# Kernel tuning notes

Measured on AMD Instinct MI355X. Metric: run time of the kernel, lower is better.

The kernel has to match this reference:

```python
import jax, jax.numpy as jnp
import numpy as np

# Frankenstein DNC dims (from __init__ defaults, L reduced 16->8 for memory budget)
X = 47764; H = 128; L = 8; VT = 3620; W = 32; R = 8; N = 512; BS = 1
D = X + R * W + 2 * H            # RNN_Unit input width = 48276
ET = W * R + 3 * W + 5 * R + 3   # interface width = 395
EPS = 1e-8


def setup_inputs() -> dict:
    key = jax.random.key(0)
    ks = jax.random.split(key, 16)
    su = 1.0 / np.sqrt(H)          # nn.Linear default-style scale
    sv = 1.0 / np.sqrt(VT)
    se = 1.0 / np.sqrt(ET)
    u = lambda k, shp, s: jax.random.uniform(k, shp, jnp.float32, -s, s)
    return {
        'x_in': jax.random.normal(ks[0], (BS, X), jnp.float32),
        # stacked per-layer LSTM-gate weights (L, D, H) / biases (L, H)
        'W_i': u(ks[1], (L, D, H), su), 'b_i': u(ks[2], (L, H), su),
        'W_f': u(ks[3], (L, D, H), su), 'b_f': u(ks[4], (L, H), su),
        'W_o': u(ks[5], (L, D, H), su), 'b_o': u(ks[6], (L, H), su),
        'W_s': u(ks[7], (L, D, H), su), 'b_s': u(ks[8], (L, H), su),
        'W_y': u(ks[9], (L * H, VT), sv),
        'W_E': u(ks[10], (L * H, ET), se),
        'W_r': u(ks[11], (W * R, VT), sv),
        # memory / state buffers (requires_grad=False in torch)
        'memory': jax.random.uniform(ks[12], (N, W), jnp.float32, -1.0, 1.0),
        'last_read_vector': jnp.zeros((BS, W, R), jnp.float32),
        'hidden_prev': jnp.zeros((BS, L, H), jnp.float32),
        'old_states': jnp.zeros((L, BS, H), jnp.float32),
        'precedence': jnp.zeros((BS, N), jnp.float32),
        'linkage': jnp.zeros((BS, N, N), jnp.float32),
        'last_read_weightings': jnp.zeros((BS, N, R), jnp.float32),
        'last_usage': jnp.zeros((BS, N), jnp.float32),
        'last_write_weighting': jnp.zeros((BS, N), jnp.float32),
    }


def reference(x_in, W_i, b_i, W_f, b_f, W_o, b_o, W_s, b_s, W_y, W_E, W_r,
              memory, last_read_vector, hidden_prev, old_states, precedence,
              linkage, last_read_weightings, last_usage, last_write_weighting):
    # ---- controller: L stacked LSTM-like units, sequential over layers ----
    input_x_t = jnp.concatenate([x_in, last_read_vector.reshape(BS, -1)], axis=1)
    hpt = jnp.transpose(hidden_prev, (1, 0, 2))  # (L, BS, H)

    def layer(h_prev_layer, xs):
        Wi, bi, Wf, bf, Wo, bo, Ws, bs_, hp, os_ = xs
        si = jnp.concatenate([input_x_t, hp, h_prev_layer], axis=1)  # (BS, D)
        ig = jax.nn.sigmoid(si @ Wi + bi)
        fg = jax.nn.sigmoid(si @ Wf + bf)
        st = fg * os_ + ig * jnp.tanh(si @ Ws + bs_)
        og = jax.nn.sigmoid(si @ Wo + bo)
        h = og * jnp.tanh(st)
        return h, h

    _, hs = jax.lax.scan(layer, jnp.zeros((BS, H), x_in.dtype),
                         (W_i, b_i, W_f, b_f, W_o, b_o, W_s, b_s, hpt, old_states))
    flat = jnp.transpose(hs, (1, 0, 2)).reshape(BS, L * H)
    output = flat @ W_y
    E = flat @ W_E

    # ---- interface vector parsing ----
    i0 = 0
    read_keys = E[:, :W * R].reshape(BS, W, R); i0 = W * R
    read_strengths = 1.0 - jax.nn.log_sigmoid(E[:, i0:i0 + R]); i0 += R
    write_key = E[:, i0:i0 + W]; i0 += W
    write_strength = 1.0 - jax.nn.log_sigmoid(E[:, i0:i0 + 1]); i0 += 1
    erase = jax.nn.sigmoid(E[:, i0:i0 + W]); i0 += W
    write_vec = E[:, i0:i0 + W]; i0 += W
    free_gates = jax.nn.sigmoid(E[:, i0:i0 + R]); i0 += R
    alloc_gate = jax.nn.sigmoid(E[:, i0:i0 + 1]); i0 += 1
    write_gate = jax.nn.sigmoid(E[:, i0:i0 + 1]); i0 += 1
    read_modes = jax.nn.softmax(E[:, i0:i0 + 3 * R].reshape(BS, R, 3), axis=2)

    # ---- memory retention, usage, allocation ----
    psi = jnp.prod(1.0 - free_gates[:, None, :] * last_read_weightings, axis=2)  # (BS,N)
    usage = (last_usage + last_write_weighting - last_usage * last_write_weighting) * psi
    idx = jnp.argsort(usage, axis=1)
    su = jnp.take_along_axis(usage, idx, axis=1)
    cp = jnp.cumprod(su, axis=1)
    excl = jnp.concatenate([jnp.ones((BS, 1), usage.dtype), cp[:, :-1]], axis=1)
    alloc = jnp.take_along_axis((1.0 - su) * excl, jnp.argsort(idx, axis=1), axis=1)

    # ---- write weighting (content + allocation) ----
    Mn = memory / jnp.maximum(jnp.linalg.norm(memory, axis=1, keepdims=True), EPS)
    kn = write_key / jnp.maximum(jnp.linalg.norm(write_key, axis=1, keepdims=True), EPS)
    cw = jax.nn.softmax(write_strength * (kn @ Mn.T), axis=1)  # (BS,N)
    ww = write_gate * (alloc_gate * alloc + (1.0 - alloc_gate) * cw)

    # ---- write to memory (bs == 1) ----
    memory_new = memory * (1.0 - jnp.einsum('bn,bw->nw', ww, erase)) \
                 + jnp.einsum('bn,bw->nw', ww, write_vec)

    # ---- temporal linkage ----
    Lm = (1.0 - ww[:, :, None] - ww[:, None, :]) * linkage \
         + ww[:, :, None] * precedence[:, None, :]
    Lm = Lm * (1.0 - jnp.eye(N, dtype=Lm.dtype))[None]
    fw = jnp.einsum('bij,bjr->bir', Lm, last_read_weightings)   # forward weighting
    bw = jnp.einsum('bji,bjr->bir', Lm, last_read_weightings)   # backward weighting

    # ---- read weightings and read vectors ----
    Mn2 = memory_new / jnp.maximum(jnp.linalg.norm(memory_new, axis=1, keepdims=True), EPS)
    knr = read_keys / jnp.maximum(jnp.linalg.norm(read_keys, axis=1, keepdims=True), EPS)
    cr = jax.nn.softmax(read_strengths[:, None, :] * jnp.einsum('nw,bwr->bnr', Mn2, knr), axis=1)
    rw = bw * read_modes[:, None, :, 0] + cr * read_modes[:, None, :, 1] \
         + fw * read_modes[:, None, :, 2]                        # (BS,N,R)
    rv = jnp.einsum('nw,bnr->bwr', memory_new, rw)               # (BS,W,R)

    y = output + rv.reshape(BS, W * R) @ W_r                     # (BS, v_t)
    return y
```

## Files before the change

kernel.cpp:

```cpp
#include <hip/hip_runtime.h>
#include <math.h>

#define XDIM 47764
#define HDIM 128
#define LDIM 8
#define VTDIM 3620
#define WDIM 32
#define RDIM 8
#define NDIM 512
#define RW 256
#define DDIM 48276
#define FIXED 48148
#define ETDIM 395
#define EPSV 1e-8f

#define CHUNK 768
#define NCHUNK 63
#define K1_COMPUTE (32 * NCHUNK)
#define K1_COPYB 128
#define KE_BLOCKS 8

#define OFF_FIXED   0
#define OFF_CNT     4096
#define OFF_WREC    262144
#define OFF_FLAT    786432
#define OFF_ERAW    787456
#define OFF_WW      787968
#define OFF_MEMNEW  788480
#define OFF_CR      804864
#define OFF_RM      808960
#define OFF_FW      808992
#define OFF_BW      813088
#define OFF_RV      817184

typedef float f4 __attribute__((ext_vector_type(4)));
typedef unsigned short us4 __attribute__((ext_vector_type(4)));

__device__ __forceinline__ f4 ntload4(const float* p) {
    return __builtin_nontemporal_load((const f4*)p);
}
__device__ __forceinline__ unsigned short f2bf(float f) {
    unsigned u = __float_as_uint(f);
    return (unsigned short)((u + 0x7FFFu + ((u >> 16) & 1u)) >> 16);
}
__device__ __forceinline__ float bf2f(unsigned short b) {
    return __uint_as_float(((unsigned)b) << 16);
}

__device__ inline float sigm(float x) { return 1.f / (1.f + expf(-x)); }
__device__ inline float log_sigmoid(float x) {
    return (x >= 0.f) ? -log1pf(expf(-x)) : (x - log1pf(expf(x)));
}

__device__ __forceinline__ bool elect_last(unsigned* cnt, unsigned total) {
    __shared__ unsigned e;
    __syncthreads();
    __threadfence();
    if (threadIdx.x == 0) e = atomicAdd(cnt, 1u);
    __syncthreads();
    if (e != total - 1) return false;
    __threadfence();
    return true;
}

__global__ __launch_bounds__(256) void k1_partial(
    const float* __restrict__ x_in, const float* __restrict__ lrv,
    const float* __restrict__ hprev,
    const float* __restrict__ Wi, const float* __restrict__ Wf,
    const float* __restrict__ Wo, const float* __restrict__ Ws,
    float* __restrict__ ws)
{
    const int bid = blockIdx.x;
    const int t   = threadIdx.x;

    if (bid >= K1_COMPUTE) {
        int cb = bid - K1_COMPUTE;
        unsigned short* wrec = (unsigned short*)(ws + OFF_WREC);
        #pragma unroll
        for (int r = 0; r < 4; ++r) {
            int idx4  = cb * 1024 + r * 256 + t;
            int flat  = idx4 << 2;
            int combo = flat >> 14;
            int rem   = flat & 16383;
            int j = rem >> 7, h = rem & 127;
            int g = combo >> 3, l = combo & 7;
            const float* Wg = (g == 0) ? Wi : (g == 1) ? Wf : (g == 2) ? Wo : Ws;
            float4 v = *reinterpret_cast<const float4*>(
                Wg + ((size_t)l * DDIM + FIXED + j) * HDIM + h);
            us4 o = { f2bf(v.x), f2bf(v.y), f2bf(v.z), f2bf(v.w) };
            *reinterpret_cast<us4*>(wrec + flat) = o;
        }
        return;
    }

    const int combo = bid / NCHUNK;
    const int chunk = bid % NCHUNK;
    const int g = combo >> 3, l = combo & 7;
    const float* __restrict__ Wg = (g == 0) ? Wi : (g == 1) ? Wf : (g == 2) ? Wo : Ws;
    const int d0 = chunk * CHUNK;

    __shared__ float s_lds[CHUNK];
    for (int i = t; i < CHUNK; i += 256) {
        int d = d0 + i;
        float v = 0.f;
        if (d < XDIM)            v = x_in[d];
        else if (d < XDIM + RW)  v = lrv[d - XDIM];
        else if (d < FIXED)      v = hprev[l * HDIM + (d - XDIM - RW)];
        s_lds[i] = v;
    }
    __syncthreads();

    const int c4 = t & 15;
    const int p  = t >> 4;
    const int r0 = p * 48;
    const float* wp = Wg + ((size_t)l * DDIM + d0 + r0) * HDIM + (c4 << 2);

    f4 a = {0.f, 0.f, 0.f, 0.f};
    f4 b = {0.f, 0.f, 0.f, 0.f};

    if (chunk != NCHUNK - 1) {
        #pragma unroll 4
        for (int i = 0; i < 48; ++i) {
            float s = s_lds[r0 + i];
            const f4 w0 = ntload4(wp);
            const f4 w1 = ntload4(wp + 64);
            wp += HDIM;
            a += s * w0;
            b += s * w1;
        }
    } else {
        for (int i = 0; i < 48; ++i) {
            if (d0 + r0 + i >= FIXED) break;
            float s = s_lds[r0 + i];
            const f4 w0 = ntload4(wp);
            const f4 w1 = ntload4(wp + 64);
            wp += HDIM;
            a += s * w0;
            b += s * w1;
        }
    }

    __shared__ f4 red[16][32];
    red[p][c4]      = a;
    red[p][c4 + 16] = b;
    __syncthreads();
    if (t < 32) {
        f4 s = red[0][t];
        #pragma unroll
        for (int q = 1; q < 16; ++q) s += red[q][t];
        float* fx = ws + OFF_FIXED + combo * HDIM + (t << 2);
        atomicAdd(fx + 0, s.x);
        atomicAdd(fx + 1, s.y);
        atomicAdd(fx + 2, s.z);
        atomicAdd(fx + 3, s.w);
    }
}

__global__ __launch_bounds__(1024) void k3_recurrent(
    const float* __restrict__ bi, const float* __restrict__ bf,
    const float* __restrict__ bo, const float* __restrict__ bs,
    const float* __restrict__ old_st, float* __restrict__ ws)
{
    const int t = threadIdx.x;
    const int g = t >> 8;
    const int q = (t >> 7) & 1;
    const int h = t & 127;
    const unsigned short* wrec = (const unsigned short*)(ws + OFF_WREC);

    __shared__ float hp[128];
    __shared__ float gl[4][2][128];

    float fx[LDIM];
    const float* bg = (g == 0) ? bi : (g == 1) ? bf : (g == 2) ? bo : bs;
    if (q == 0) {
        #pragma unroll
        for (int l = 0; l < LDIM; ++l)
            fx[l] = ws[OFF_FIXED + (g * 8 + l) * HDIM + h] + bg[l * HDIM + h];
    }
    if (t < 128) hp[t] = 0.f;
    __syncthreads();

    for (int l = 0; l < LDIM; ++l) {
        int combo = g * 8 + l;
        float acc = (q == 0) ? fx[l] : 0.f;
        const unsigned short* wr = wrec + (size_t)combo * 16384 + (q << 6) * 128 + h;
        #pragma unroll 8
        for (int j = 0; j < 64; ++j)
            acc += hp[(q << 6) + j] * bf2f(wr[j * 128]);
        gl[g][q][h] = acc;
        __syncthreads();
        if (t < 128) {
            float ig = sigm(gl[0][0][t] + gl[0][1][t]);
            float fg = sigm(gl[1][0][t] + gl[1][1][t]);
            float og = sigm(gl[2][0][t] + gl[2][1][t]);
            float ss = tanhf(gl[3][0][t] + gl[3][1][t]);
            float st = fg * old_st[l * HDIM + t] + ig * ss;
            float hn = og * tanhf(st);
            hp[t] = hn;
            ws[OFF_FLAT + l * HDIM + t] = hn;
        }
        __syncthreads();
    }
}

__global__ __launch_bounds__(512) void kE6(
    const float* __restrict__ We,
    const float* __restrict__ memory, const float* __restrict__ lrw,
    const float* __restrict__ lu, const float* __restrict__ lww,
    float* __restrict__ ws)
{
    const int blk = blockIdx.x, t = threadIdx.x;
    const int lane = t & 63, wid = t >> 6;

    {
        __shared__ float flat_s[1024];
        __shared__ float pr[512];
        flat_s[t]       = ws[OFF_FLAT + t];
        flat_s[512 + t] = ws[OFF_FLAT + 512 + t];
        __syncthreads();
        const int ks = t >> 6, e64 = t & 63;
        const int e = blk * 64 + e64;
        float acc = 0.f;
        if (e < ETDIM) {
            const float* Wp = We + (size_t)(ks * 128) * ETDIM + e;
            #pragma unroll 8
            for (int k = 0; k < 128; ++k)
                acc += flat_s[ks * 128 + k] * Wp[(size_t)k * ETDIM];
        }
        pr[ks * 64 + e64] = acc;
        __syncthreads();
        if (t < 64) {
            int ee = blk * 64 + t;
            if (ee < ETDIM) {
                float s = 0.f;
                #pragma unroll
                for (int qq = 0; qq < 8; ++qq) s += pr[qq * 64 + t];
                ws[OFF_ERAW + ee] = s;
            }
        }
    }

    if (!elect_last((unsigned*)(ws + OFF_CNT), KE_BLOCKS)) return;
    __syncthreads();

    __shared__ float Es[416], rk[256], wk[32], er[32], wvv[32];
    __shared__ float fgs[8], rss[8], rm[24], scal[4], u_s[512];
    __shared__ float wred[8], wred8[64], srk[8];

    if (t < ETDIM) Es[t] = ws[OFF_ERAW + t];
    if (t < 256) ws[OFF_RV + t] = 0.f;
    __syncthreads();

    if (t < 256)                 rk[t] = Es[t];
    if (t >= 256 && t < 264)     rss[t - 256] = 1.f - log_sigmoid(Es[t]);
    if (t >= 264 && t < 296)     wk[t - 264] = Es[t];
    if (t == 296)                scal[0] = 1.f - log_sigmoid(Es[296]);
    if (t >= 297 && t < 329)     er[t - 297] = sigm(Es[t]);
    if (t >= 329 && t < 361)     wvv[t - 329] = Es[t];
    if (t >= 361 && t < 369)     fgs[t - 361] = sigm(Es[t]);
    if (t == 369)                scal[1] = sigm(Es[369]);
    if (t == 370)                scal[2] = sigm(Es[370]);
    if (t >= 384 && t < 392) {
        int r = t - 384;
        float a = Es[371 + 3*r], b = Es[372 + 3*r], c = Es[373 + 3*r];
        float mx = fmaxf(a, fmaxf(b, c));
        float ea = expf(a - mx), eb = expf(b - mx), ec = expf(c - mx);
        float s = ea + eb + ec;
        rm[3*r] = ea / s; rm[3*r + 1] = eb / s; rm[3*r + 2] = ec / s;
    }
    __syncthreads();

    float psi = 1.f;
    #pragma unroll
    for (int r = 0; r < 8; ++r) psi *= 1.f - fgs[r] * lrw[t * 8 + r];
    float ua = lu[t], ub = lww[t];
    float u_t = (ua + ub - ua * ub) * psi;
    u_s[t] = u_t;
    __syncthreads();

    float prod = 1.f;
    for (int j = 0; j < 512; ++j) {
        float uj = u_s[j];
        bool before = (uj < u_t) || (uj == u_t && j < t);
        prod *= before ? uj : 1.f;
    }
    float alloc_t = (1.f - u_t) * prod;

    float s2 = 0.f;
    #pragma unroll
    for (int w = 0; w < 32; ++w) s2 += wk[w] * wk[w];
    float wkinv = 1.f / fmaxf(sqrtf(s2), EPSV);

    float mrow[32];
    float dotv = 0.f, nn = 0.f;
    #pragma unroll
    for (int w = 0; w < 32; ++w) {
        float m = memory[t * 32 + w];
        mrow[w] = m; dotv += m * wk[w]; nn += m * m;
    }
    float score = scal[0] * wkinv * dotv / fmaxf(sqrtf(nn), EPSV);
    float v = score;
    #pragma unroll
    for (int o = 32; o > 0; o >>= 1) v = fmaxf(v, __shfl_xor(v, o));
    if (lane == 0) wred[wid] = v;
    __syncthreads();
    float mx = wred[0];
    #pragma unroll
    for (int qq = 1; qq < 8; ++qq) mx = fmaxf(mx, wred[qq]);
    __syncthreads();
    float e = expf(score - mx);
    v = e;
    #pragma unroll
    for (int o = 32; o > 0; o >>= 1) v += __shfl_xor(v, o);
    if (lane == 0) wred[wid] = v;
    __syncthreads();
    float ssum = 0.f;
    #pragma unroll
    for (int qq = 0; qq < 8; ++qq) ssum += wred[qq];
    float cwv = e / ssum;

    float wwn = scal[2] * (scal[1] * alloc_t + (1.f - scal[1]) * cwv);
    ws[OFF_WW + t] = wwn;

    float nn2 = 0.f;
    #pragma unroll
    for (int w = 0; w < 32; ++w) {
        float mn = mrow[w] * (1.f - wwn * er[w]) + wwn * wvv[w];
        mrow[w] = mn; nn2 += mn * mn;
        ws[OFF_MEMNEW + t * 32 + w] = mn;
    }
    float inv2 = 1.f / fmaxf(sqrtf(nn2), EPSV);

    if (t < 8) {
        float s3 = 0.f;
        #pragma unroll
        for (int w = 0; w < 32; ++w) { float x = rk[w * 8 + t]; s3 += x * x; }
        srk[t] = rss[t] / fmaxf(sqrtf(s3), EPSV);
    }
    __syncthreads();

    float sc[8];
    #pragma unroll
    for (int r = 0; r < 8; ++r) {
        float d2 = 0.f;
        #pragma unroll
        for (int w = 0; w < 32; ++w) d2 += mrow[w] * rk[w * 8 + r];
        sc[r] = srk[r] * inv2 * d2;
    }
    #pragma unroll
    for (int r = 0; r < 8; ++r) {
        float x = sc[r];
        #pragma unroll
        for (int o = 32; o > 0; o >>= 1) x = fmaxf(x, __shfl_xor(x, o));
        if (lane == 0) wred8[wid * 8 + r] = x;
    }
    __syncthreads();
    float mxr[8];
    #pragma unroll
    for (int r = 0; r < 8; ++r) {
        float m = wred8[r];
        #pragma unroll
        for (int qq = 1; qq < 8; ++qq) m = fmaxf(m, wred8[qq * 8 + r]);
        mxr[r] = m;
    }
    __syncthreads();
    float ex[8];
    #pragma unroll
    for (int r = 0; r < 8; ++r) {
        ex[r] = expf(sc[r] - mxr[r]);
        float x = ex[r];
        #pragma unroll
        for (int o = 32; o > 0; o >>= 1) x += __shfl_xor(x, o);
        if (lane == 0) wred8[wid * 8 + r] = x;
    }
    __syncthreads();
    #pragma unroll
    for (int r = 0; r < 8; ++r) {
        float sm = 0.f;
        #pragma unroll
        for (int qq = 0; qq < 8; ++qq) sm += wred8[qq * 8 + r];
        ws[OFF_CR + t * 8 + r] = ex[r] / sm;
    }
    if (t < 24) ws[OFF_RM + t] = rm[t];
}

__global__ __launch_bounds__(512) void k7_linkage(
    const float* __restrict__ linkage, const float* __restrict__ prec,
    const float* __restrict__ lrw, float* __restrict__ ws)
{
    const int blk = blockIdx.x, t = threadIdx.x;
    const int lane = t & 63, wid = t >> 6;
    __shared__ float lrw_s[4608];
    __shared__ float ww_s[512];
    __shared__ float rowred[64];
    __shared__ float fwbw_s[2][2][8];

    for (int i = t; i < 4096; i += 512)
        lrw_s[(i >> 3) * 9 + (i & 7)] = lrw[i];
    ww_s[t] = ws[OFF_WW + t];
    __syncthreads();

    const float pt = prec[t];
    const float wwt = ww_s[t];
    float la[8];
    #pragma unroll
    for (int r = 0; r < 8; ++r) la[r] = lrw_s[t * 9 + r];

    #pragma unroll
    for (int pass = 0; pass < 4; ++pass) {
        const int i = blk * 2 + (pass & 1);
        float lm;
        if (pass < 2) {
            float lj = linkage[(size_t)i * 512 + t];
            lm = (t == i) ? 0.f : (1.f - ww_s[i] - wwt) * lj + ww_s[i] * pt;
        } else {
            float lj = linkage[(size_t)t * 512 + i];
            lm = (t == i) ? 0.f : (1.f - wwt - ww_s[i]) * lj + wwt * prec[i];
        }
        #pragma unroll
        for (int r = 0; r < 8; ++r) {
            float v = lm * la[r];
            #pragma unroll
            for (int o = 32; o > 0; o >>= 1) v += __shfl_xor(v, o);
            if (lane == 0) rowred[wid * 8 + r] = v;
        }
        __syncthreads();
        if (t < 8) {
            float s = 0.f;
            #pragma unroll
            for (int w = 0; w < 8; ++w) s += rowred[w * 8 + t];
            ws[((pass < 2) ? OFF_FW : OFF_BW) + i * 8 + t] = s;
            fwbw_s[pass >> 1][pass & 1][t] = s;
        }
        __syncthreads();
    }

    if (t < 256) {
        const int w = t >> 3, r = t & 7;
        const float rm0 = ws[OFF_RM + r * 3];
        const float rm1 = ws[OFF_RM + r * 3 + 1];
        const float rm2 = ws[OFF_RM + r * 3 + 2];
        float val = 0.f;
        #pragma unroll
        for (int p2 = 0; p2 < 2; ++p2) {
            int n = blk * 2 + p2;
            float rwn = fwbw_s[1][p2][r] * rm0
                      + ws[OFF_CR + n * 8 + r] * rm1
                      + fwbw_s[0][p2][r] * rm2;
            val += ws[OFF_MEMNEW + n * 32 + w] * rwn;
        }
        atomicAdd(&ws[OFF_RV + t], val);
    }
}

__global__ __launch_bounds__(512) void kout(
    const float* __restrict__ Wy, const float* __restrict__ Wr,
    float* __restrict__ dout, const float* __restrict__ ws)
{
    const int blk = blockIdx.x, t = threadIdx.x;
    __shared__ float flat_s[1024];
    __shared__ float rv_s[256];
    __shared__ float pr[512];
    flat_s[t]       = ws[OFF_FLAT + t];
    flat_s[512 + t] = ws[OFF_FLAT + 512 + t];
    if (t < 256) rv_s[t] = ws[OFF_RV + t];
    __syncthreads();

    const int ks = t >> 4, v16 = t & 15;
    const int v = blk * 16 + v16;
    float acc = 0.f;
    if (v < VTDIM) {
        const float* Wp = Wy + (size_t)(ks * 32) * VTDIM + v;
        #pragma unroll 8
        for (int k = 0; k < 32; ++k)
            acc += flat_s[ks * 32 + k] * Wp[(size_t)k * VTDIM];
        const float* Wp2 = Wr + (size_t)(ks * 8) * VTDIM + v;
        #pragma unroll
        for (int k = 0; k < 8; ++k)
            acc += rv_s[ks * 8 + k] * Wp2[(size_t)k * VTDIM];
    }
    pr[ks * 16 + v16] = acc;
    __syncthreads();
    if (t < 16) {
        int vv = blk * 16 + t;
        if (vv < VTDIM) {
            float s = 0.f;
            #pragma unroll
            for (int q = 0; q < 32; ++q) s += pr[q * 16 + t];
            dout[vv] = s;
        }
    }
}

extern "C" void kernel_launch(void* const* d_in, const int* in_sizes, int n_in,
                              void* d_out, int out_size, void* d_ws, size_t ws_size,
                              hipStream_t stream)
{
    const float* x_in   = (const float*)d_in[0];
    const float* Wi     = (const float*)d_in[1];
    const float* bi     = (const float*)d_in[2];
    const float* Wf     = (const float*)d_in[3];
    const float* bf     = (const float*)d_in[4];
    const float* Wo     = (const float*)d_in[5];
    const float* bo     = (const float*)d_in[6];
    const float* Wss    = (const float*)d_in[7];
    const float* bs     = (const float*)d_in[8];
    const float* Wy     = (const float*)d_in[9];
    const float* We     = (const float*)d_in[10];
    const float* Wr     = (const float*)d_in[11];
    const float* memory = (const float*)d_in[12];
    const float* lrv    = (const float*)d_in[13];
    const float* hprev  = (const float*)d_in[14];
    const float* old_st = (const float*)d_in[15];
    const float* prec   = (const float*)d_in[16];
    const float* linkage= (const float*)d_in[17];
    const float* lrw    = (const float*)d_in[18];
    const float* lu     = (const float*)d_in[19];
    const float* lww    = (const float*)d_in[20];
    float* out = (float*)d_out;
    float* ws  = (float*)d_ws;

    hipMemsetAsync((void*)ws, 0, (4096 + 4) * sizeof(float), stream);

    k1_partial<<<K1_COMPUTE + K1_COPYB, 256, 0, stream>>>(
        x_in, lrv, hprev, Wi, Wf, Wo, Wss, ws);
    k3_recurrent<<<1, 1024, 0, stream>>>(bi, bf, bo, bs, old_st, ws);
    kE6<<<KE_BLOCKS, 512, 0, stream>>>(We, memory, lrw, lu, lww, ws);
    k7_linkage<<<256, 512, 0, stream>>>(linkage, prec, lrw, ws);
    kout<<<227, 512, 0, stream>>>(Wy, Wr, out, ws);
}
```

Before: 240.6 us.

## Fuse recurrent, interface, linkage and output kernels into one persistent tail kernel

Replaces the four tail launches (recurrent LSTM, interface/memory, linkage, output) with a single 256-block kernel that uses global flags and an atomic counter as grid-wide barriers. Blocks other than the recurrent block wait on a flag, then split the interface projection and the W_y projection across block ranges, while W_r is applied at the end via atomicAdd into the output. The goal is to remove kernel launch gaps and overlap the W_y GEMV with the memory-addressing work. It depends on all 256 blocks being co-resident for the spin waits, and the atomic output accumulation changes the summation order.

After: 363.8 us. +51.2%, slower.

```diff
diff --git a/kernel.cpp b/kernel.cpp
--- a/kernel.cpp
+++ b/kernel.cpp
@@ -18,10 +18,12 @@
 #define NCHUNK 63
 #define K1_COMPUTE (32 * NCHUNK)
 #define K1_COPYB 128
-#define KE_BLOCKS 8
 
 #define OFF_FIXED   0
-#define OFF_CNT     4096
+#define OFF_FLAGA   4096
+#define OFF_FLAGB   4097
+#define OFF_CNTC    4098
+#define OFF_CNTE    4099
 #define OFF_WREC    262144
 #define OFF_FLAT    786432
 #define OFF_ERAW    787456
@@ -52,6 +54,17 @@
     return (x >= 0.f) ? -log1pf(expf(-x)) : (x - log1pf(expf(x)));
 }
 
+__device__ __forceinline__ void set_flag(unsigned* f) {
+    __syncthreads();
+    __threadfence();
+    if (threadIdx.x == 0) atomicExch(f, 1u);
+}
+__device__ __forceinline__ void wait_flag(unsigned* f) {
+    if (threadIdx.x == 0)
+        while (atomicAdd(f, 0u) == 0u) __builtin_amdgcn_s_sleep(64);
+    __syncthreads();
+    __threadfence();
+}
 __device__ __forceinline__ bool elect_last(unsigned* cnt, unsigned total) {
     __shared__ unsigned e;
     __syncthreads();
@@ -156,338 +169,352 @@
     }
 }
 
-__global__ __launch_bounds__(1024) void k3_recurrent(
+__global__ __launch_bounds__(512) void big_tail(
     const float* __restrict__ bi, const float* __restrict__ bf,
     const float* __restrict__ bo, const float* __restrict__ bs,
-    const float* __restrict__ old_st, float* __restrict__ ws)
+    const float* __restrict__ old_st,
+    const float* __restrict__ Wy, const float* __restrict__ We,
+    const float* __restrict__ Wr,
+    const float* __restrict__ memory, const float* __restrict__ lrw,
+    const float* __restrict__ lu, const float* __restrict__ lww,
+    const float* __restrict__ linkage, const float* __restrict__ prec,
+    float* __restrict__ ws, float* __restrict__ out)
 {
-    const int t = threadIdx.x;
-    const int g = t >> 8;
-    const int q = (t >> 7) & 1;
-    const int h = t & 127;
+    const int blk = blockIdx.x, t = threadIdx.x;
+    const int lane = t & 63, wid = t >> 6;
+    unsigned* flagA = (unsigned*)(ws + OFF_FLAGA);
+    unsigned* flagB = (unsigned*)(ws + OFF_FLAGB);
+    unsigned* cntC  = (unsigned*)(ws + OFF_CNTC);
+    unsigned* cntE  = (unsigned*)(ws + OFF_CNTE);
     const unsigned short* wrec = (const unsigned short*)(ws + OFF_WREC);
 
-    __shared__ float hp[128];
-    __shared__ float gl[4][2][128];
-
-    float fx[LDIM];
-    const float* bg = (g == 0) ? bi : (g == 1) ? bf : (g == 2) ? bo : bs;
-    if (q == 0) {
+    if (blk == 0) {
+        __shared__ float hp[128];
+        __shared__ float gl[4][128];
+        const int g = t >> 7, h = t & 127;
+        float fx[LDIM];
+        const float* bg = (g == 0) ? bi : (g == 1) ? bf : (g == 2) ? bo : bs;
         #pragma unroll
         for (int l = 0; l < LDIM; ++l)
             fx[l] = ws[OFF_FIXED + (g * 8 + l) * HDIM + h] + bg[l * HDIM + h];
-    }
-    if (t < 128) hp[t] = 0.f;
-    __syncthreads();
-
-    for (int l = 0; l < LDIM; ++l) {
-        int combo = g * 8 + l;
-        float acc = (q == 0) ? fx[l] : 0.f;
-        const unsigned short* wr = wrec + (size_t)combo * 16384 + (q << 6) * 128 + h;
-        #pragma unroll 8
-        for (int j = 0; j < 64; ++j)
-            acc += hp[(q << 6) + j] * bf2f(wr[j * 128]);
-        gl[g][q][h] = acc;
+        if (t < 128) hp[t] = 0.f;
         __syncthreads();
-        if (t < 128) {
-            float ig = sigm(gl[0][0][t] + gl[0][1][t]);
-            float fg = sigm(gl[1][0][t] + gl[1][1][t]);
-            float og = sigm(gl[2][0][t] + gl[2][1][t]);
-            float ss = tanhf(gl[3][0][t] + gl[3][1][t]);
-            float st = fg * old_st[l * HDIM + t] + ig * ss;
-            float hn = og * tanhf(st);
-            hp[t] = hn;
-            ws[OFF_FLAT + l * HDIM + t] = hn;
-        }
-        __syncthreads();
-    }
-}
-
-__global__ __launch_bounds__(512) void kE6(
-    const float* __restrict__ We,
-    const float* __restrict__ memory, const float* __restrict__ lrw,
-    const float* __restrict__ lu, const float* __restrict__ lww,
-    float* __restrict__ ws)
-{
-    const int blk = blockIdx.x, t = threadIdx.x;
-    const int lane = t & 63, wid = t >> 6;
-
-    {
+
+        for (int l = 0; l < LDIM; ++l) {
+            int combo = g * 8 + l;
+            float acc = fx[l];
+            const unsigned short* wr = wrec + (size_t)combo * 16384 + h;
+            #pragma unroll 16
+            for (int j = 0; j < 128; ++j)
+                acc += hp[j] * bf2f(wr[j * 128]);
+            gl[g][h] = acc;
+            __syncthreads();
+            if (t < 128) {
+                float ig = sigm(gl[0][t]);
+                float fg = sigm(gl[1][t]);
+                float og = sigm(gl[2][t]);
+                float ss = tanhf(gl[3][t]);
+                float st = fg * old_st[l * HDIM + t] + ig * ss;
+                float hn = og * tanhf(st);
+                hp[t] = hn;
+                ws[OFF_FLAT + l * HDIM + t] = hn;
+            }
+            __syncthreads();
+        }
+        set_flag(flagA);
+    } else {
+        wait_flag(flagA);
+    }
+
+    if (blk < 8) {
+        {
+            __shared__ float flat_s[1024];
+            __shared__ float pr[512];
+            flat_s[t]       = ws[OFF_FLAT + t];
+            flat_s[512 + t] = ws[OFF_FLAT + 512 + t];
+            __syncthreads();
+            const int ks = t >> 6, e64 = t & 63;
+            const int e = blk * 64 + e64;
+            float acc = 0.f;
+            if (e < ETDIM) {
+                const float* Wp = We + (size_t)(ks * 128) * ETDIM + e;
+                #pragma unroll 8
+                for (int k = 0; k < 128; ++k)
+                    acc += flat_s[ks * 128 + k] * Wp[(size_t)k * ETDIM];
+            }
+            pr[ks * 64 + e64] = acc;
+            __syncthreads();
+            if (t < 64) {
+                int ee = blk * 64 + t;
+                if (ee < ETDIM) {
+                    float s = 0.f;
+                    #pragma unroll
+                    for (int qq = 0; qq < 8; ++qq) s += pr[qq * 64 + t];
+                    ws[OFF_ERAW + ee] = s;
+                }
+            }
+        }
+
+        if (elect_last(cntE, 8)) {
+            __shared__ float Es[416], rk[256], wk[32], er[32], wvv[32];
+            __shared__ float fgs[8], rss[8], rm[24], scal[4], u_s[512];
+            __shared__ float wred[8], wred8[64], srk[8];
+
+            if (t < ETDIM) Es[t] = ws[OFF_ERAW + t];
+            if (t < 256) ws[OFF_RV + t] = 0.f;
+            __syncthreads();
+
+            if (t < 256)                 rk[t] = Es[t];
+            if (t >= 256 && t < 264)     rss[t - 256] = 1.f - log_sigmoid(Es[t]);
+            if (t >= 264 && t < 296)     wk[t - 264] = Es[t];
+            if (t == 296)                scal[0] = 1.f - log_sigmoid(Es[296]);
+            if (t >= 297 && t < 329)     er[t - 297] = sigm(Es[t]);
+            if (t >= 329 && t < 361)     wvv[t - 329] = Es[t];
+            if (t >= 361 && t < 369)     fgs[t - 361] = sigm(Es[t]);
+            if (t == 369)                scal[1] = sigm(Es[369]);
+            if (t == 370)                scal[2] = sigm(Es[370]);
+            if (t >= 384 && t < 392) {
+                int r = t - 384;
+                float a = Es[371 + 3*r], b = Es[372 + 3*r], c = Es[373 + 3*r];
+                float mx = fmaxf(a, fmaxf(b, c));
+                float ea = expf(a - mx), eb = expf(b - mx), ec = expf(c - mx);
+                float s = ea + eb + ec;
+                rm[3*r] = ea / s; rm[3*r + 1] = eb / s; rm[3*r + 2] = ec / s;
+            }
+            __syncthreads();
+
+            float psi = 1.f;
+            #pragma unroll
+            for (int r = 0; r < 8; ++r) psi *= 1.f - fgs[r] * lrw[t * 8 + r];
+            float ua = lu[t], ub = lww[t];
+            float u_t = (ua + ub - ua * ub) * psi;
+            u_s[t] = u_t;
+            __syncthreads();
+
+            float prod = 1.f;
+            for (int j = 0; j < 512; ++j) {
+                float uj = u_s[j];
+                bool before = (uj < u_t) || (uj == u_t && j < t);
+                prod *= before ? uj : 1.f;
+            }
+            float alloc_t = (1.f - u_t) * prod;
+
+            float s2 = 0.f;
+            #pragma unroll
+            for (int w = 0; w < 32; ++w) s2 += wk[w] * wk[w];
+            float wkinv = 1.f / fmaxf(sqrtf(s2), EPSV);
+
+            float mrow[32];
+            float dotv = 0.f, nn = 0.f;
+            #pragma unroll
+            for (int w = 0; w < 32; ++w) {
+                float m = memory[t * 32 + w];
+                mrow[w] = m; dotv += m * wk[w]; nn += m * m;
+            }
+            float score = scal[0] * wkinv * dotv / fmaxf(sqrtf(nn), EPSV);
+            float v = score;
+            #pragma unroll
+            for (int o = 32; o > 0; o >>= 1) v = fmaxf(v, __shfl_xor(v, o));
+            if (lane == 0) wred[wid] = v;
+            __syncthreads();
+            float mx = wred[0];
+            #pragma unroll
+            for (int qq = 1; qq < 8; ++qq) mx = fmaxf(mx, wred[qq]);
+            __syncthreads();
+            float e = expf(score - mx);
+            v = e;
+            #pragma unroll
+            for (int o = 32; o > 0; o >>= 1) v += __shfl_xor(v, o);
+            if (lane == 0) wred[wid] = v;
+            __syncthreads();
+            float ssum = 0.f;
+            #pragma unroll
+            for (int qq = 0; qq < 8; ++qq) ssum += wred[qq];
+            float cwv = e / ssum;
+
+            float wwn = scal[2] * (scal[1] * alloc_t + (1.f - scal[1]) * cwv);
+            ws[OFF_WW + t] = wwn;
+
+            float nn2 = 0.f;
+            #pragma unroll
+            for (int w = 0; w < 32; ++w) {
+                float mn = mrow[w] * (1.f - wwn * er[w]) + wwn * wvv[w];
+                mrow[w] = mn; nn2 += mn * mn;
+                ws[OFF_MEMNEW + t * 32 + w] = mn;
+            }
+            float inv2 = 1.f / fmaxf(sqrtf(nn2), EPSV);
+
+            if (t < 8) {
+                float s3 = 0.f;
+                #pragma unroll
+                for (int w = 0; w < 32; ++w) { float x = rk[w * 8 + t]; s3 += x * x; }
+                srk[t] = rss[t] / fmaxf(sqrtf(s3), EPSV);
+            }
+            __syncthreads();
+
+            float sc[8];
+            #pragma unroll
+            for (int r = 0; r < 8; ++r) {
+                float d2 = 0.f;
+                #pragma unroll
+                for (int w = 0; w < 32; ++w) d2 += mrow[w] * rk[w * 8 + r];
+                sc[r] = srk[r] * inv2 * d2;
+            }
+            #pragma unroll
+            for (int r = 0; r < 8; ++r) {
+                float x = sc[r];
+                #pragma unroll
+                for (int o = 32; o > 0; o >>= 1) x = fmaxf(x, __shfl_xor(x, o));
+                if (lane == 0) wred8[wid * 8 + r] = x;
+            }
+            __syncthreads();
+            float mxr[8];
+            #pragma unroll
+            for (int r = 0; r < 8; ++r) {
+                float m = wred8[r];
+                #pragma unroll
+                for (int qq = 1; qq < 8; ++qq) m = fmaxf(m, wred8[qq * 8 + r]);
+                mxr[r] = m;
+            }
+            __syncthreads();
+            float ex[8];
+            #pragma unroll
+            for (int r = 0; r < 8; ++r) {
+                ex[r] = expf(sc[r] - mxr[r]);
+                float x = ex[r];
+                #pragma unroll
+                for (int o = 32; o > 0; o >>= 1) x += __shfl_xor(x, o);
+                if (lane == 0) wred8[wid * 8 + r] = x;
+            }
+            __syncthreads();
+            #pragma unroll
+            for (int r = 0; r < 8; ++r) {
+                float sm = 0.f;
+                #pragma unroll
+                for (int qq = 0; qq < 8; ++qq) sm += wred8[qq * 8 + r];
+                ws[OFF_CR + t * 8 + r] = ex[r] / sm;
+            }
+            if (t < 24) ws[OFF_RM + t] = rm[t];
+
+            set_flag(flagB);
+        }
+    } else if (blk < 235) {
         __shared__ float flat_s[1024];
         __shared__ float pr[512];
         flat_s[t]       = ws[OFF_FLAT + t];
         flat_s[512 + t] = ws[OFF_FLAT + 512 + t];
         __syncthreads();
-        const int ks = t >> 6, e64 = t & 63;
-        const int e = blk * 64 + e64;
+        const int ks = t >> 4, v16 = t & 15;
+        const int v = (blk - 8) * 16 + v16;
         float acc = 0.f;
-        if (e < ETDIM) {
-            const float* Wp = We + (size_t)(ks * 128) * ETDIM + e;
+        if (v < VTDIM) {
+            const float* Wp = Wy + (size_t)(ks * 32) * VTDIM + v;
             #pragma unroll 8
-            for (int k = 0; k < 128; ++k)
-                acc += flat_s[ks * 128 + k] * Wp[(size_t)k * ETDIM];
-        }
-        pr[ks * 64 + e64] = acc;
+            for (int k = 0; k < 32; ++k)
+                acc += flat_s[ks * 32 + k] * Wp[(size_t)k * VTDIM];
+        }
+        pr[ks * 16 + v16] = acc;
         __syncthreads();
-        if (t < 64) {
-            int ee = blk * 64 + t;
-            if (ee < ETDIM) {
+        if (t < 16) {
+            int vv = (blk - 8) * 16 + t;
+            if (vv < VTDIM) {
                 float s = 0.f;
                 #pragma unroll
-                for (int qq = 0; qq < 8; ++qq) s += pr[qq * 64 + t];
-                ws[OFF_ERAW + ee] = s;
-            }
-        }
-    }
-
-    if (!elect_last((unsigned*)(ws + OFF_CNT), KE_BLOCKS)) return;
-    __syncthreads();
-
-    __shared__ float Es[416], rk[256], wk[32], er[32], wvv[32];
-    __shared__ float fgs[8], rss[8], rm[24], scal[4], u_s[512];
-    __shared__ float wred[8], wred8[64], srk[8];
-
-    if (t < ETDIM) Es[t] = ws[OFF_ERAW + t];
-    if (t < 256) ws[OFF_RV + t] = 0.f;
-    __syncthreads();
-
-    if (t < 256)                 rk[t] = Es[t];
-    if (t >= 256 && t < 264)     rss[t - 256] = 1.f - log_sigmoid(Es[t]);
-    if (t >= 264 && t < 296)     wk[t - 264] = Es[t];
-    if (t == 296)                scal[0] = 1.f - log_sigmoid(Es[296]);
-    if (t >= 297 && t < 329)     er[t - 297] = sigm(Es[t]);
-    if (t >= 329 && t < 361)     wvv[t - 329] = Es[t];
-    if (t >= 361 && t < 369)     fgs[t - 361] = sigm(Es[t]);
-    if (t == 369)                scal[1] = sigm(Es[369]);
-    if (t == 370)                scal[2] = sigm(Es[370]);
-    if (t >= 384 && t < 392) {
-        int r = t - 384;
-        float a = Es[371 + 3*r], b = Es[372 + 3*r], c = Es[373 + 3*r];
-        float mx = fmaxf(a, fmaxf(b, c));
-        float ea = expf(a - mx), eb = expf(b - mx), ec = expf(c - mx);
-        float s = ea + eb + ec;
-        rm[3*r] = ea / s; rm[3*r + 1] = eb / s; rm[3*r + 2] = ec / s;
-    }
-    __syncthreads();
-
-    float psi = 1.f;
-    #pragma unroll
-    for (int r = 0; r < 8; ++r) psi *= 1.f - fgs[r] * lrw[t * 8 + r];
-    float ua = lu[t], ub = lww[t];
-    float u_t = (ua + ub - ua * ub) * psi;
-    u_s[t] = u_t;
-    __syncthreads();
-
-    float prod = 1.f;
-    for (int j = 0; j < 512; ++j) {
-        float uj = u_s[j];
-        bool before = (uj < u_t) || (uj == u_t && j < t);
-        prod *= before ? uj : 1.f;
-    }
-    float alloc_t = (1.f - u_t) * prod;
-
-    float s2 = 0.f;
-    #pragma unroll
-    for (int w = 0; w < 32; ++w) s2 += wk[w] * wk[w];
-    float wkinv = 1.f / fmaxf(sqrtf(s2), EPSV);
-
-    float mrow[32];
-    float dotv = 0.f, nn = 0.f;
-    #pragma unroll
-    for (int w = 0; w < 32; ++w) {
-        float m = memory[t * 32 + w];
-        mrow[w] = m; dotv += m * wk[w]; nn += m * m;
-    }
-    float score = scal[0] * wkinv * dotv / fmaxf(sqrtf(nn), EPSV);
-    float v = score;
-    #pragma unroll
-    for (int o = 32; o > 0; o >>= 1) v = fmaxf(v, __shfl_xor(v, o));
-    if (lane == 0) wred[wid] = v;
-    __syncthreads();
-    float mx = wred[0];
-    #pragma unroll
-    for (int qq = 1; qq < 8; ++qq) mx = fmaxf(mx, wred[qq]);
-    __syncthreads();
-    float e = expf(score - mx);
-    v = e;
-    #pragma unroll
-    for (int o = 32; o > 0; o >>= 1) v += __shfl_xor(v, o);
-    if (lane == 0) wred[wid] = v;
-    __syncthreads();
-    float ssum = 0.f;
-    #pragma unroll
-    for (int qq = 0; qq < 8; ++qq) ssum += wred[qq];
-    float cwv = e / ssum;
-
-    float wwn = scal[2] * (scal[1] * alloc_t + (1.f - scal[1]) * cwv);
-    ws[OFF_WW + t] = wwn;
-
-    float nn2 = 0.f;
-    #pragma unroll
-    for (int w = 0; w < 32; ++w) {
-        float mn = mrow[w] * (1.f - wwn * er[w]) + wwn * wvv[w];
-        mrow[w] = mn; nn2 += mn * mn;
-        ws[OFF_MEMNEW + t * 32 + w] = mn;
-    }
-    float inv2 = 1.f / fmaxf(sqrtf(nn2), EPSV);
-
-    if (t < 8) {
-        float s3 = 0.f;
+                for (int q = 0; q < 32; ++q) s += pr[q * 16 + t];
+                out[vv] = s;
+            }
+        }
+    }
+
+    wait_flag(flagB);
+
+    {
+        __shared__ float lrw_s[4608];
+        __shared__ float ww_s[512];
+        __shared__ float rowred[64];
+        __shared__ float fwbw_s[2][2][8];
+
+        for (int i = t; i < 4096; i += 512)
+            lrw_s[(i >> 3) * 9 + (i & 7)] = lrw[i];
+        ww_s[t] = ws[OFF_WW + t];
+        __syncthreads();
+
+        const float pt = prec[t];
+        const float wwt = ww_s[t];
+        float la[8];
         #pragma unroll
-        for (int w = 0; w < 32; ++w) { float x = rk[w * 8 + t]; s3 += x * x; }
-        srk[t] = rss[t] / fmaxf(sqrtf(s3), EPSV);
-    }
-    __syncthreads();
-
-    float sc[8];
-    #pragma unroll
-    for (int r = 0; r < 8; ++r) {
-        float d2 = 0.f;
+        for (int r = 0; r < 8; ++r) la[r] = lrw_s[t * 9 + r];
+
         #pragma unroll
-        for (int w = 0; w < 32; ++w) d2 += mrow[w] * rk[w * 8 + r];
-        sc[r] = srk[r] * inv2 * d2;
-    }
-    #pragma unroll
-    for (int r = 0; r < 8; ++r) {
-        float x = sc[r];
-        #pragma unroll
-        for (int o = 32; o > 0; o >>= 1) x = fmaxf(x, __shfl_xor(x, o));
-        if (lane == 0) wred8[wid * 8 + r] = x;
-    }
-    __syncthreads();
-    float mxr[8];
-    #pragma unroll
-    for (int r = 0; r < 8; ++r) {
-        float m = wred8[r];
-        #pragma unroll
-        for (int qq = 1; qq < 8; ++qq) m = fmaxf(m, wred8[qq * 8 + r]);
-        mxr[r] = m;
-    }
-    __syncthreads();
-    float ex[8];
-    #pragma unroll
-    for (int r = 0; r < 8; ++r) {
-        ex[r] = expf(sc[r] - mxr[r]);
-        float x = ex[r];
-        #pragma unroll
-        for (int o = 32; o > 0; o >>= 1) x += __shfl_xor(x, o);
-        if (lane == 0) wred8[wid * 8 + r] = x;
-    }
-    __syncthreads();
-    #pragma unroll
-    for (int r = 0; r < 8; ++r) {
-        float sm = 0.f;
-        #pragma unroll
-        for (int qq = 0; qq < 8; ++qq) sm += wred8[qq * 8 + r];
-        ws[OFF_CR + t * 8 + r] = ex[r] / sm;
-    }
-    if (t < 24) ws[OFF_RM + t] = rm[t];
-}
-
-__global__ __launch_bounds__(512) void k7_linkage(
-    const float* __restrict__ linkage, const float* __restrict__ prec,
-    const float* __restrict__ lrw, float* __restrict__ ws)
-{
-    const int blk = blockIdx.x, t = threadIdx.x;
-    const int lane = t & 63, wid = t >> 6;
-    __shared__ float lrw_s[4608];
-    __shared__ float ww_s[512];
-    __shared__ float rowred[64];
-    __shared__ float fwbw_s[2][2][8];
-
-    for (int i = t; i < 4096; i += 512)
-        lrw_s[(i >> 3) * 9 + (i & 7)] = lrw[i];
-    ww_s[t] = ws[OFF_WW + t];
-    __syncthreads();
-
-    const float pt = prec[t];
-    const float wwt = ww_s[t];
-    float la[8];
-    #pragma unroll
-    for (int r = 0; r < 8; ++r) la[r] = lrw_s[t * 9 + r];
-
-    #pragma unroll
-    for (int pass = 0; pass < 4; ++pass) {
-        const int i = blk * 2 + (pass & 1);
-        float lm;
-        if (pass < 2) {
-            float lj = linkage[(size_t)i * 512 + t];
-            lm = (t == i) ? 0.f : (1.f - ww_s[i] - wwt) * lj + ww_s[i] * pt;
-        } else {
-            float lj = linkage[(size_t)t * 512 + i];
-            lm = (t == i) ? 0.f : (1.f - wwt - ww_s[i]) * lj + wwt * prec[i];
-        }
-        #pragma unroll
-        for (int r = 0; r < 8; ++r) {
-            float v = lm * la[r];
-            #pragma unroll
-            for (int o = 32; o > 0; o >>= 1) v += __shfl_xor(v, o);
-            if (lane == 0) rowred[wid * 8 + r] = v;
-        }
+        for (int pass = 0; pass < 4; ++pass) {
+            const int i = blk * 2 + (pass & 1);
+            float lm;
+            if (pass < 2) {
+                float lj = linkage[(size_t)i * 512 + t];
+                lm = (t == i) ? 0.f : (1.f - ww_s[i] - wwt) * lj + ww_s[i] * pt;
+            } else {
+                float lj = linkage[(size_t)t * 512 + i];
+                lm = (t == i) ? 0.f : (1.f - wwt - ww_s[i]) * lj + wwt * prec[i];
+            }
+            #pragma unroll
+            for (int r = 0; r < 8; ++r) {
+                float v = lm * la[r];
+                #pragma unroll
+                for (int o = 32; o > 0; o >>= 1) v += __shfl_xor(v, o);
+                if (lane == 0) rowred[wid * 8 + r] = v;
+            }
+            __syncthreads();
+            if (t < 8) {
+                float s = 0.f;
+                #pragma unroll
+                for (int w = 0; w < 8; ++w) s += rowred[w * 8 + t];
+                fwbw_s[pass >> 1][pass & 1][t] = s;
+            }
+            __syncthreads();
+        }
+
+        if (t < 256) {
+            const int w = t >> 3, r = t & 7;
+            const float rm0 = ws[OFF_RM + r * 3];
+            const float rm1 = ws[OFF_RM + r * 3 + 1];
+            const float rm2 = ws[OFF_RM + r * 3 + 2];
+            float val = 0.f;
+            #pragma unroll
+            for (int p2 = 0; p2 < 2; ++p2) {
+                int n = blk * 2 + p2;
+                float rwn = fwbw_s[1][p2][r] * rm0
+                          + ws[OFF_CR + n * 8 + r] * rm1
+                          + fwbw_s[0][p2][r] * rm2;
+                val += ws[OFF_MEMNEW + n * 32 + w] * rwn;
+            }
+            atomicAdd(&ws[OFF_RV + t], val);
+        }
+    }
+
+    __syncthreads();
+    __threadfence();
+    if (t == 0) {
+        atomicAdd(cntC, 1u);
+        while (atomicAdd(cntC, 0u) < 256u) __builtin_amdgcn_s_sleep(32);
+    }
+    __syncthreads();
+    __threadfence();
+
+    if (blk < 60) {
+        __shared__ float rv_s[64];
+        const int vt = blk % 15, kc = blk / 15;
+        if (t < 64) rv_s[t] = ws[OFF_RV + kc * 64 + t];
         __syncthreads();
-        if (t < 8) {
-            float s = 0.f;
-            #pragma unroll
-            for (int w = 0; w < 8; ++w) s += rowred[w * 8 + t];
-            ws[((pass < 2) ? OFF_FW : OFF_BW) + i * 8 + t] = s;
-            fwbw_s[pass >> 1][pass & 1][t] = s;
-        }
-        __syncthreads();
-    }
-
-    if (t < 256) {
-        const int w = t >> 3, r = t & 7;
-        const float rm0 = ws[OFF_RM + r * 3];
-        const float rm1 = ws[OFF_RM + r * 3 + 1];
-        const float rm2 = ws[OFF_RM + r * 3 + 2];
-        float val = 0.f;
-        #pragma unroll
-        for (int p2 = 0; p2 < 2; ++p2) {
-            int n = blk * 2 + p2;
-            float rwn = fwbw_s[1][p2][r] * rm0
-                      + ws[OFF_CR + n * 8 + r] * rm1
-                      + fwbw_s[0][p2][r] * rm2;
-            val += ws[OFF_MEMNEW + n * 32 + w] * rwn;
-        }
-        atomicAdd(&ws[OFF_RV + t], val);
-    }
-}
-
-__global__ __launch_bounds__(512) void kout(
-    const float* __restrict__ Wy, const float* __restrict__ Wr,
-    float* __restrict__ dout, const float* __restrict__ ws)
-{
-    const int blk = blockIdx.x, t = threadIdx.x;
-    __shared__ float flat_s[1024];
-    __shared__ float rv_s[256];
-    __shared__ float pr[512];
-    flat_s[t]       = ws[OFF_FLAT + t];
-    flat_s[512 + t] = ws[OFF_FLAT + 512 + t];
-    if (t < 256) rv_s[t] = ws[OFF_RV + t];
-    __syncthreads();
-
-    const int ks = t >> 4, v16 = t & 15;
-    const int v = blk * 16 + v16;
-    float acc = 0.f;
-    if (v < VTDIM) {
-        const float* Wp = Wy + (size_t)(ks * 32) * VTDIM + v;
-        #pragma unroll 8
-        for (int k = 0; k < 32; ++k)
-            acc += flat_s[ks * 32 + k] * Wp[(size_t)k * VTDIM];
-        const float* Wp2 = Wr + (size_t)(ks * 8) * VTDIM + v;
-        #pragma unroll
-        for (int k = 0; k < 8; ++k)
-            acc += rv_s[ks * 8 + k] * Wp2[(size_t)k * VTDIM];
-    }
-    pr[ks * 16 + v16] = acc;
-    __syncthreads();
-    if (t < 16) {
-        int vv = blk * 16 + t;
-        if (vv < VTDIM) {
-            float s = 0.f;
-            #pragma unroll
-            for (int q = 0; q < 32; ++q) s += pr[q * 16 + t];
-            dout[vv] = s;
+        if (t < 256) {
+            int v = vt * 256 + t;
+            if (v < VTDIM) {
+                float acc = 0.f;
+                const float* Wp = Wr + (size_t)kc * 64 * VTDIM + v;
+                #pragma unroll 8
+                for (int k = 0; k < 64; ++k)
+                    acc += rv_s[k] * Wp[(size_t)k * VTDIM];
+                atomicAdd(&out[v], acc);
+            }
         }
     }
 }
@@ -520,12 +547,12 @@
     float* out = (float*)d_out;
     float* ws  = (float*)d_ws;
 
-    hipMemsetAsync((void*)ws, 0, (4096 + 4) * sizeof(float), stream);
+    hipMemsetAsync((void*)ws, 0, (4096 + 8) * sizeof(float), stream);
 
     k1_partial<<<K1_COMPUTE + K1_COPYB, 256, 0, stream>>>(
         x_in, lrv, hprev, Wi, Wf, Wo, Wss, ws);
-    k3_recurrent<<<1, 1024, 0, stream>>>(bi, bf, bo, bs, old_st, ws);
-    kE6<<<KE_BLOCKS, 512, 0, stream>>>(We, memory, lrw, lu, lww, ws);
-    k7_linkage<<<256, 512, 0, stream>>>(linkage, prec, lrw, ws);
-    kout<<<227, 512, 0, stream>>>(Wy, Wr, out, ws);
-}
+
+    big_tail<<<256, 512, 0, stream>>>(
+        bi, bf, bo, bs, old_st, Wy, We, Wr,
+        memory, lrw, lu, lww, linkage, prec, ws, out);
+}
```

## Fuse recurrent LSTM kernel into interface kernel with flag-based block synchronization

Applied to the files above, without the earlier changes.

Moves the sequential 8-layer recurrent LSTM step into block 0 of the interface kernel, while the other blocks spin-wait on a global flag. This removes one kernel launch and its gap. The recurrent matvec now runs with 512 threads instead of 1024, each loading 8 bf16 weights as one vector and reducing partial sums through shared memory. It also stops writing the forward/backward weightings to global memory. The spin-wait relies on all 8 blocks being co-resident, and the memset must still clear the new flag and counter words.

New measurement: 254.0 us. 1.06x slower.

```diff
diff --git a/kernel.cpp b/kernel.cpp
--- a/kernel.cpp
+++ b/kernel.cpp
@@ -21,7 +21,8 @@
 #define KE_BLOCKS 8
 
 #define OFF_FIXED   0
-#define OFF_CNT     4096
+#define OFF_FLAGA   4096
+#define OFF_CNTE    4097
 #define OFF_WREC    262144
 #define OFF_FLAT    786432
 #define OFF_ERAW    787456
@@ -35,6 +36,7 @@
 
 typedef float f4 __attribute__((ext_vector_type(4)));
 typedef unsigned short us4 __attribute__((ext_vector_type(4)));
+typedef unsigned short us8 __attribute__((ext_vector_type(8)));
 
 __device__ __forceinline__ f4 ntload4(const float* p) {
     return __builtin_nontemporal_load((const f4*)p);
@@ -52,6 +54,17 @@
     return (x >= 0.f) ? -log1pf(expf(-x)) : (x - log1pf(expf(x)));
 }
 
+__device__ __forceinline__ void set_flag(unsigned* f) {
+    __syncthreads();
+    __threadfence();
+    if (threadIdx.x == 0) atomicExch(f, 1u);
+}
+__device__ __forceinline__ void wait_flag(unsigned* f) {
+    if (threadIdx.x == 0)
+        while (atomicAdd(f, 0u) == 0u) __builtin_amdgcn_s_sleep(64);
+    __syncthreads();
+    __threadfence();
+}
 __device__ __forceinline__ bool elect_last(unsigned* cnt, unsigned total) {
     __shared__ unsigned e;
     __syncthreads();
@@ -156,54 +169,10 @@
     }
 }
 
-__global__ __launch_bounds__(1024) void k3_recurrent(
+__global__ __launch_bounds__(512) void kE6(
     const float* __restrict__ bi, const float* __restrict__ bf,
     const float* __restrict__ bo, const float* __restrict__ bs,
-    const float* __restrict__ old_st, float* __restrict__ ws)
-{
-    const int t = threadIdx.x;
-    const int g = t >> 8;
-    const int q = (t >> 7) & 1;
-    const int h = t & 127;
-    const unsigned short* wrec = (const unsigned short*)(ws + OFF_WREC);
-
-    __shared__ float hp[128];
-    __shared__ float gl[4][2][128];
-
-    float fx[LDIM];
-    const float* bg = (g == 0) ? bi : (g == 1) ? bf : (g == 2) ? bo : bs;
-    if (q == 0) {
-        #pragma unroll
-        for (int l = 0; l < LDIM; ++l)
-            fx[l] = ws[OFF_FIXED + (g * 8 + l) * HDIM + h] + bg[l * HDIM + h];
-    }
-    if (t < 128) hp[t] = 0.f;
-    __syncthreads();
-
-    for (int l = 0; l < LDIM; ++l) {
-        int combo = g * 8 + l;
-        float acc = (q == 0) ? fx[l] : 0.f;
-        const unsigned short* wr = wrec + (size_t)combo * 16384 + (q << 6) * 128 + h;
-        #pragma unroll 8
-        for (int j = 0; j < 64; ++j)
-            acc += hp[(q << 6) + j] * bf2f(wr[j * 128]);
-        gl[g][q][h] = acc;
-        __syncthreads();
-        if (t < 128) {
-            float ig = sigm(gl[0][0][t] + gl[0][1][t]);
-            float fg = sigm(gl[1][0][t] + gl[1][1][t]);
-            float og = sigm(gl[2][0][t] + gl[2][1][t]);
-            float ss = tanhf(gl[3][0][t] + gl[3][1][t]);
-            float st = fg * old_st[l * HDIM + t] + ig * ss;
-            float hn = og * tanhf(st);
-            hp[t] = hn;
-            ws[OFF_FLAT + l * HDIM + t] = hn;
-        }
-        __syncthreads();
-    }
-}
-
-__global__ __launch_bounds__(512) void kE6(
+    const float* __restrict__ old_st,
     const float* __restrict__ We,
     const float* __restrict__ memory, const float* __restrict__ lrw,
     const float* __restrict__ lu, const float* __restrict__ lww,
@@ -211,6 +180,72 @@
 {
     const int blk = blockIdx.x, t = threadIdx.x;
     const int lane = t & 63, wid = t >> 6;
+    unsigned* flagA = (unsigned*)(ws + OFF_FLAGA);
+    unsigned* cntE  = (unsigned*)(ws + OFF_CNTE);
+    const unsigned short* wrec = (const unsigned short*)(ws + OFF_WREC);
+
+    if (blk == 0) {
+        __shared__ float hp[128];
+        __shared__ float gl4[4][128];
+        __shared__ float redc[4][8][132];
+
+        const int g  = t >> 7;
+        const int w  = t & 127;
+        const int hb = w >> 3;
+        const int js = w & 7;
+        const int h  = w;
+
+        float fx[LDIM];
+        const float* bg = (g == 0) ? bi : (g == 1) ? bf : (g == 2) ? bo : bs;
+        #pragma unroll
+        for (int l = 0; l < LDIM; ++l)
+            fx[l] = ws[OFF_FIXED + (g * 8 + l) * HDIM + h] + bg[l * HDIM + h];
+
+        if (t < 128) hp[t] = 0.f;
+        __syncthreads();
+
+        for (int l = 0; l < LDIM; ++l) {
+            const int combo = g * 8 + l;
+            const unsigned short* wb = wrec + (size_t)combo * 16384 + hb * 8;
+            float acc[8] = {0, 0, 0, 0, 0, 0, 0, 0};
+            #pragma unroll
+            for (int jj = 0; jj < 16; ++jj) {
+                const int j = js * 16 + jj;
+                us8 wv = *reinterpret_cast<const us8*>(wb + j * 128);
+                const float hj = hp[j];
+                acc[0] += hj * bf2f(wv[0]);
+                acc[1] += hj * bf2f(wv[1]);
+                acc[2] += hj * bf2f(wv[2]);
+                acc[3] += hj * bf2f(wv[3]);
+                acc[4] += hj * bf2f(wv[4]);
+                acc[5] += hj * bf2f(wv[5]);
+                acc[6] += hj * bf2f(wv[6]);
+                acc[7] += hj * bf2f(wv[7]);
+            }
+            #pragma unroll
+            for (int i = 0; i < 8; ++i) redc[g][js][hb * 8 + i] = acc[i];
+            __syncthreads();
+            float s = fx[l];
+            #pragma unroll
+            for (int q2 = 0; q2 < 8; ++q2) s += redc[g][q2][h];
+            gl4[g][h] = s;
+            __syncthreads();
+            if (t < 128) {
+                float ig = sigm(gl4[0][t]);
+                float fg = sigm(gl4[1][t]);
+                float og = sigm(gl4[2][t]);
+                float ss = tanhf(gl4[3][t]);
+                float st = fg * old_st[l * HDIM + t] + ig * ss;
+                float hn = og * tanhf(st);
+                hp[t] = hn;
+                ws[OFF_FLAT + l * HDIM + t] = hn;
+            }
+            __syncthreads();
+        }
+        set_flag(flagA);
+    } else {
+        wait_flag(flagA);
+    }
 
     {
         __shared__ float flat_s[1024];
@@ -240,7 +275,7 @@
         }
     }
 
-    if (!elect_last((unsigned*)(ws + OFF_CNT), KE_BLOCKS)) return;
+    if (!elect_last(cntE, KE_BLOCKS)) return;
     __syncthreads();
 
     __shared__ float Es[416], rk[256], wk[32], er[32], wvv[32];
@@ -429,7 +464,6 @@
             float s = 0.f;
             #pragma unroll
             for (int w = 0; w < 8; ++w) s += rowred[w * 8 + t];
-            ws[((pass < 2) ? OFF_FW : OFF_BW) + i * 8 + t] = s;
             fwbw_s[pass >> 1][pass & 1][t] = s;
         }
         __syncthreads();
@@ -524,8 +558,8 @@
 
     k1_partial<<<K1_COMPUTE + K1_COPYB, 256, 0, stream>>>(
         x_in, lrv, hprev, Wi, Wf, Wo, Wss, ws);
-    k3_recurrent<<<1, 1024, 0, stream>>>(bi, bf, bo, bs, old_st, ws);
-    kE6<<<KE_BLOCKS, 512, 0, stream>>>(We, memory, lrw, lu, lww, ws);
+    kE6<<<KE_BLOCKS, 512, 0, stream>>>(
+        bi, bf, bo, bs, old_st, We, memory, lrw, lu, lww, ws);
     k7_linkage<<<256, 512, 0, stream>>>(linkage, prec, lrw, ws);
     kout<<<227, 512, 0, stream>>>(Wy, Wr, out, ws);
 }
```
